# Optimization experiments

Hardware: AMD Instinct MI355X
Metric: run time of the kernel (lower is better)

The kernel has to match this reference:

```python
import jax, jax.numpy as jnp
import numpy as np
from jax import lax

START, STOP, NTAGS = 18, 19, 20
NEG = -10000.0
V, E, H, L = 100000, 300, 512, 512  # vocab, embed_dim, per-direction hidden, seq_len


def setup_inputs() -> dict:
    key = jax.random.key(0)
    ks = jax.random.split(key, 16)
    f = lambda k, s: jax.random.normal(k, s, dtype=jnp.float32) * 0.05
    trans = jax.random.normal(ks[14], (NTAGS, NTAGS), dtype=jnp.float32)
    trans = trans.at[START, :].set(NEG).at[:, STOP].set(NEG)
    return {
        "sentence": jax.random.randint(ks[0], (L,), 0, V),
        "embed_table": f(ks[1], (V, E)),
        "w_ih_f": f(ks[2], (4 * H, E)), "w_hh_f": f(ks[3], (4 * H, H)),
        "b_ih_f": f(ks[4], (4 * H,)), "b_hh_f": f(ks[5], (4 * H,)),
        "w_ih_b": f(ks[6], (4 * H, E)), "w_hh_b": f(ks[7], (4 * H, H)),
        "b_ih_b": f(ks[8], (4 * H,)), "b_hh_b": f(ks[9], (4 * H,)),
        "h0": f(ks[10], (2, H)), "c0": f(ks[11], (2, H)),
        "w_out": f(ks[12], (NTAGS, 2 * H)), "b_out": f(ks[13], (NTAGS,)),
        "transitions": trans,
    }


def _lstm_dir(x, wih, whh, bih, bhh, h0, c0, reverse):
    # x: [L, E]; PyTorch gate order i, f, g, o
    b = bih + bhh
    def step(carry, xt):
        h, c = carry
        g = xt @ wih.T + h @ whh.T + b  # [4H]
        i, fg, gg, o = jnp.split(g, 4)
        c = jax.nn.sigmoid(fg) * c + jax.nn.sigmoid(i) * jnp.tanh(gg)
        h = jax.nn.sigmoid(o) * jnp.tanh(c)
        return (h, c), h
    _, hs = lax.scan(step, (h0, c0), x, reverse=reverse)
    return hs  # [L, H] in time order


def _lstm_feats(sentence, embed_table, w_ih_f, w_hh_f, b_ih_f, b_hh_f,
                w_ih_b, w_hh_b, b_ih_b, b_hh_b, h0, c0, w_out, b_out):
    x = embed_table[sentence]  # [L, E]
    hf = _lstm_dir(x, w_ih_f, w_hh_f, b_ih_f, b_hh_f, h0[0], c0[0], False)
    hb = _lstm_dir(x, w_ih_b, w_hh_b, b_ih_b, b_hh_b, h0[1], c0[1], True)
    h = jnp.concatenate([hf, hb], axis=-1)  # [L, 2H]
    return h @ w_out.T + b_out  # [L, NTAGS]


def reference(sentence, embed_table, w_ih_f, w_hh_f, b_ih_f, b_hh_f,
              w_ih_b, w_hh_b, b_ih_b, b_hh_b, h0, c0, w_out, b_out, transitions):
    feats = _lstm_feats(sentence, embed_table, w_ih_f, w_hh_f, b_ih_f, b_hh_f,
                        w_ih_b, w_hh_b, b_ih_b, b_hh_b, h0, c0, w_out, b_out)
    init = jnp.full((NTAGS,), NEG, dtype=feats.dtype).at[START].set(0.0)

    def vstep(fv, feat):
        scores = fv[None, :] + transitions  # [next_tag, prev_tag]
        bptr = jnp.argmax(scores, axis=1)
        return jnp.max(scores, axis=1) + feat, bptr

    fv, bptrs = lax.scan(vstep, init, feats)  # bptrs: [L, NTAGS]
    terminal = fv + transitions[STOP]
    best = jnp.argmax(terminal)

    def back(tag, bp):
        # tag is the best tag at step t; bp maps tag_t -> tag_{t-1}
        return bp[tag], tag

    _, path = lax.scan(back, best, bptrs, reverse=True)  # [L] in time order
    return path
```

## Files before the change

kernel.cpp:

```cpp
#include <hip/hip_runtime.h>
#include <math.h>

#define L 512
#define E 300
#define H 512
#define G4H 2048
#define NTAGS 20
#define START_TAG 18
#define STOP_TAG 19

#define GPD 32
#define HPW 16
#define TR  16

#define OFF_XW    0u
#define OFF_HIST  8388608u
#define OFF_HBUF  10485760u
#define OFF_FEATS 10502144u

__global__ void k1_xw(const int* __restrict__ sentence,
                      const float* __restrict__ embed,
                      const float* __restrict__ wih_f, const float* __restrict__ wih_b,
                      const float* __restrict__ bih_f, const float* __restrict__ bhh_f,
                      const float* __restrict__ bih_b, const float* __restrict__ bhh_b,
                      float* __restrict__ xw) {
    int tid = threadIdx.x;
    int n   = blockIdx.x * 256 + tid;
    int t0  = blockIdx.y * TR;
    int dir = blockIdx.z;
    const float* wih = dir ? wih_b : wih_f;
    const float* bih = dir ? bih_b : bih_f;
    const float* bhh = dir ? bhh_b : bhh_f;
    const float* wrow = wih + (size_t)n * E;

    const float* xr[TR];
#pragma unroll
    for (int r = 0; r < TR; ++r)
        xr[r] = embed + (size_t)sentence[t0 + r] * E;

    float acc[TR];
#pragma unroll
    for (int r = 0; r < TR; ++r) acc[r] = 0.f;

    for (int kk = 0; kk < E / 4; ++kk) {
        float4 wv = ((const float4*)wrow)[kk];
#pragma unroll
        for (int r = 0; r < TR; ++r) {
            float4 xv = ((const float4*)xr[r])[kk];
            acc[r] = fmaf(wv.x, xv.x,
                     fmaf(wv.y, xv.y,
                     fmaf(wv.z, xv.z,
                     fmaf(wv.w, xv.w, acc[r]))));
        }
    }
    float b = bih[n] + bhh[n];
#pragma unroll
    for (int r = 0; r < TR; ++r)
        xw[((size_t)(dir * L) + (t0 + r)) * G4H + n] = acc[r] + b;
}

__global__ __launch_bounds__(512) void k2_lstm(
    const float* __restrict__ whh_f, const float* __restrict__ whh_b,
    const float* __restrict__ h0, const float* __restrict__ c0,
    const float* __restrict__ xw, float* __restrict__ hist,
    unsigned long long* __restrict__ hbuf) {
    const int bid = blockIdx.x;
    const int dir = bid >> 5;
    const int wg  = bid & 31;
    const int tid = threadIdx.x;
    const int wv  = tid >> 6;
    const int l   = tid & 63;
    const int gate = l >> 4;
    const int j    = l & 15;
    const int row  = gate * H + wg * HPW + j;

    const float* whh = dir ? whh_b : whh_f;
    const float* xwd = xw + (size_t)dir * L * G4H;
    float* histd = hist + (size_t)dir * L * H;
    unsigned long long* hb = hbuf + dir * 1024;

    float w[64];
    {
        const float* wp = whh + (size_t)row * H + wv * 64;
#pragma unroll
        for (int i = 0; i < 64; i += 4) {
            float4 v = *(const float4*)(wp + i);
            w[i] = v.x; w[i + 1] = v.y; w[i + 2] = v.z; w[i + 3] = v.w;
        }
    }

    __shared__ float pbuf[2][8][64];

    float c = (tid < HPW) ? c0[dir * H + wg * HPW + tid] : 0.f;

    for (int s = 1; s <= L; ++s) {
        const int t = dir ? (L - s) : (s - 1);
        float xg = xwd[(size_t)t * G4H + row];

        float hval;
        if (s == 1) {
            hval = h0[dir * H + tid];
        } else {
            unsigned long long* slot = hb + (((s - 1) & 1) << 9) + tid;
            unsigned long long u;
            while (((u = __hip_atomic_load(slot, __ATOMIC_RELAXED,
                                           __HIP_MEMORY_SCOPE_AGENT)) >> 32)
                   != (unsigned)(s - 1))
                __builtin_amdgcn_s_sleep(1);
            hval = __uint_as_float((unsigned)u);
        }

        float acc = 0.f;
#pragma unroll
        for (int i = 0; i < 64; ++i) {
            float hb_i = __uint_as_float(
                (unsigned)__builtin_amdgcn_readlane((int)__float_as_uint(hval), i));
            acc = fmaf(w[i], hb_i, acc);
        }
        pbuf[s & 1][wv][l] = acc;
        __syncthreads();

        if (tid < 64) {
            float g = 0.f;
#pragma unroll
            for (int p = 0; p < 8; ++p) g += pbuf[s & 1][p][l];
            float pre = g + xg;
            float a  = (gate == 2) ? 2.f * pre : pre;
            float sg = 1.f / (1.f + __expf(-a));
            float v  = (gate == 2) ? (2.f * sg - 1.f) : sg;
            float ig = __shfl(v, j);
            float fg = __shfl(v, j + 16);
            float gg = __shfl(v, j + 32);
            float og = __shfl(v, j + 48);
            if (tid < HPW) {
                c = fg * c + ig * gg;
                float tc = 2.f / (1.f + __expf(-2.f * c)) - 1.f;
                float h  = og * tc;
                histd[(size_t)t * H + wg * HPW + tid] = h;
                unsigned long long u =
                    ((unsigned long long)(unsigned)s << 32) |
                    (unsigned long long)__float_as_uint(h);
                __hip_atomic_store(hb + ((s & 1) << 9) + wg * HPW + tid, u,
                                   __ATOMIC_RELAXED, __HIP_MEMORY_SCOPE_AGENT);
            }
        }
    }
}

__global__ void k3_feats(const float* __restrict__ hist,
                         const float* __restrict__ wout,
                         const float* __restrict__ bout,
                         float* __restrict__ feats) {
    int t = blockIdx.x;
    int tid = threadIdx.x;
    int tag = tid >> 4;
    int part = tid & 15;
    const float* h0p = hist + (size_t)t * H;
    const float* h1p = hist + (size_t)L * H + (size_t)t * H;
    int j0 = part * 64;
    float acc = 0.f;
    for (int jj = 0; jj < 64; jj += 4) {
        int j = j0 + jj;
        float4 w4 = *(const float4*)(wout + (size_t)tag * (2 * H) + j);
        float4 h4 = (j < H) ? *(const float4*)(h0p + j)
                            : *(const float4*)(h1p + (j - H));
        acc = fmaf(w4.x, h4.x, fmaf(w4.y, h4.y,
              fmaf(w4.z, h4.z, fmaf(w4.w, h4.w, acc))));
    }
    acc += __shfl_xor(acc, 8, 16);
    acc += __shfl_xor(acc, 4, 16);
    acc += __shfl_xor(acc, 2, 16);
    acc += __shfl_xor(acc, 1, 16);
    if (part == 0) feats[(size_t)t * NTAGS + tag] = acc + bout[tag];
}

__global__ void k4_viterbi(const float* __restrict__ feats,
                           const float* __restrict__ trans,
                           int* __restrict__ out) {
    __shared__ unsigned char bp[L * NTAGS];
    int lane = threadIdx.x;
    bool act = lane < NTAGS;

    float trl[NTAGS];
#pragma unroll
    for (int p = 0; p < NTAGS; ++p)
        trl[p] = act ? trans[lane * NTAGS + p] : -1.0e30f;

    float fv = (lane == START_TAG) ? 0.f : -10000.f;
    float nf = act ? feats[lane] : 0.f;

    for (int t = 0; t < L; ++t) {
        float f = nf;
        if (act && t + 1 < L) nf = feats[(size_t)(t + 1) * NTAGS + lane];
        float best = -1.0e30f;
        int b = 0;
#pragma unroll
        for (int p = 0; p < NTAGS; ++p) {
            float sc = __shfl(fv, p) + trl[p];
            if (sc > best) { best = sc; b = p; }
        }
        fv = best + f;
        if (act) bp[t * NTAGS + lane] = (unsigned char)b;
    }

    float ts = act ? fv + trans[STOP_TAG * NTAGS + lane] : -1.0e30f;
    int bi = lane;
#pragma unroll
    for (int off = 32; off; off >>= 1) {
        float ov = __shfl_down(ts, off);
        int   oi = __shfl_down(bi, off);
        if (ov > ts) { ts = ov; bi = oi; }
    }
    if (lane == 0) {
        int tag = bi;
        out[L - 1] = tag;
        for (int t = L - 1; t >= 1; --t) {
            tag = bp[t * NTAGS + tag];
            out[t - 1] = tag;
        }
    }
}

extern "C" void kernel_launch(void* const* d_in, const int* in_sizes, int n_in,
                              void* d_out, int out_size, void* d_ws, size_t ws_size,
                              hipStream_t stream) {
    const int*   sentence = (const int*)d_in[0];
    const float* embed    = (const float*)d_in[1];
    const float* wih_f    = (const float*)d_in[2];
    const float* whh_f    = (const float*)d_in[3];
    const float* bih_f    = (const float*)d_in[4];
    const float* bhh_f    = (const float*)d_in[5];
    const float* wih_b    = (const float*)d_in[6];
    const float* whh_b    = (const float*)d_in[7];
    const float* bih_b    = (const float*)d_in[8];
    const float* bhh_b    = (const float*)d_in[9];
    const float* h0       = (const float*)d_in[10];
    const float* c0       = (const float*)d_in[11];
    const float* wout     = (const float*)d_in[12];
    const float* bout     = (const float*)d_in[13];
    const float* trans    = (const float*)d_in[14];
    int* out = (int*)d_out;

    char* ws = (char*)d_ws;
    float* xw    = (float*)(ws + OFF_XW);
    float* hist  = (float*)(ws + OFF_HIST);
    float* feats = (float*)(ws + OFF_FEATS);
    unsigned long long* hbuf = (unsigned long long*)(ws + OFF_HBUF);

    k1_xw<<<dim3(8, 32, 2), 256, 0, stream>>>(sentence, embed, wih_f, wih_b,
                                              bih_f, bhh_f, bih_b, bhh_b, xw);
    {
        void* args[] = {(void*)&whh_f, (void*)&whh_b, (void*)&h0, (void*)&c0,
                        (void*)&xw, (void*)&hist, (void*)&hbuf};
        hipLaunchCooperativeKernel((const void*)k2_lstm, dim3(2 * GPD), dim3(512),
                                   args, 0, stream);
    }
    k3_feats<<<L, 320, 0, stream>>>(hist, wout, bout, feats);
    k4_viterbi<<<1, 64, 0, stream>>>(feats, trans, out);
}
```

Before: 1.498 ms.

## Restructure LSTM recurrence into 256 single-wave blocks handling both directions

The recurrent kernel now uses 256 single-wavefront blocks. Each block owns two hidden units for both directions and keeps both directions' recurrent weights in registers. Hidden state is exchanged through tagged 64-bit slots polled in bulk, and the cross-wave shared-memory reduction and __syncthreads are replaced by in-wave shuffles. The input projection stages embeddings in shared memory with a smaller row tile and writes gate-interleaved output, and the Viterbi argmax becomes a tree reduction. The aim is to shorten the per-timestep critical path. The trade-offs are that every block now polls for all 512 hidden values per direction, and the cooperative launch is dropped, so co-residency of all 256 blocks is assumed rather than guaranteed.

```diff
diff --git a/kernel.cpp b/kernel.cpp
--- a/kernel.cpp
+++ b/kernel.cpp
@@ -1,5 +1,8 @@
 #include <hip/hip_runtime.h>
 #include <math.h>
+
+typedef unsigned long long u64;
+typedef unsigned int u32;
 
 #define L 512
 #define E 300
@@ -9,9 +12,7 @@
 #define START_TAG 18
 #define STOP_TAG 19
 
-#define GPD 32
-#define HPW 16
-#define TR  16
+#define TR 8
 
 #define OFF_XW    0u
 #define OFF_HIST  8388608u
@@ -24,6 +25,7 @@
                       const float* __restrict__ bih_f, const float* __restrict__ bhh_f,
                       const float* __restrict__ bih_b, const float* __restrict__ bhh_b,
                       float* __restrict__ xw) {
+    __shared__ float xs[TR][304];
     int tid = threadIdx.x;
     int n   = blockIdx.x * 256 + tid;
     int t0  = blockIdx.y * TR;
@@ -31,13 +33,13 @@
     const float* wih = dir ? wih_b : wih_f;
     const float* bih = dir ? bih_b : bih_f;
     const float* bhh = dir ? bhh_b : bhh_f;
+
+    for (int r = 0; r < TR; ++r)
+        for (int k = tid; k < E; k += 256)
+            xs[r][k] = embed[(size_t)sentence[t0 + r] * E + k];
+    __syncthreads();
+
     const float* wrow = wih + (size_t)n * E;
-
-    const float* xr[TR];
-#pragma unroll
-    for (int r = 0; r < TR; ++r)
-        xr[r] = embed + (size_t)sentence[t0 + r] * E;
-
     float acc[TR];
 #pragma unroll
     for (int r = 0; r < TR; ++r) acc[r] = 0.f;
@@ -46,103 +48,164 @@
         float4 wv = ((const float4*)wrow)[kk];
 #pragma unroll
         for (int r = 0; r < TR; ++r) {
-            float4 xv = ((const float4*)xr[r])[kk];
-            acc[r] = fmaf(wv.x, xv.x,
-                     fmaf(wv.y, xv.y,
-                     fmaf(wv.z, xv.z,
-                     fmaf(wv.w, xv.w, acc[r]))));
+            float4 xv = *(const float4*)(&xs[r][kk * 4]);
+            acc[r] = fmaf(wv.x, xv.x, fmaf(wv.y, xv.y,
+                     fmaf(wv.z, xv.z, fmaf(wv.w, xv.w, acc[r]))));
         }
     }
     float b = bih[n] + bhh[n];
+    int u = n & (H - 1), gate = n >> 9;
+    int pos = (u >> 1) * 8 + gate * 2 + (u & 1);
 #pragma unroll
     for (int r = 0; r < TR; ++r)
-        xw[((size_t)(dir * L) + (t0 + r)) * G4H + n] = acc[r] + b;
-}
-
-__global__ __launch_bounds__(512) void k2_lstm(
+        xw[((size_t)(dir * L) + (t0 + r)) * G4H + pos] = acc[r] + b;
+}
+
+__global__ __launch_bounds__(64) void k2_lstm(
     const float* __restrict__ whh_f, const float* __restrict__ whh_b,
     const float* __restrict__ h0, const float* __restrict__ c0,
     const float* __restrict__ xw, float* __restrict__ hist,
-    unsigned long long* __restrict__ hbuf) {
-    const int bid = blockIdx.x;
-    const int dir = bid >> 5;
-    const int wg  = bid & 31;
-    const int tid = threadIdx.x;
-    const int wv  = tid >> 6;
-    const int l   = tid & 63;
-    const int gate = l >> 4;
-    const int j    = l & 15;
-    const int row  = gate * H + wg * HPW + j;
-
-    const float* whh = dir ? whh_b : whh_f;
-    const float* xwd = xw + (size_t)dir * L * G4H;
-    float* histd = hist + (size_t)dir * L * H;
-    unsigned long long* hb = hbuf + dir * 1024;
-
-    float w[64];
+    u64* __restrict__ hbuf) {
+    const int g2 = blockIdx.x;
+    const int l  = threadIdx.x;
+    const int j  = l & 7;
+    const int q  = l >> 3;
+    const int u0 = g2 * 2;
+    const int row = (j >> 1) * H + u0 + (j & 1);
+
+    float w0[64], w1[64];
     {
-        const float* wp = whh + (size_t)row * H + wv * 64;
+        const float* p0 = whh_f + (size_t)row * H + q * 64;
+        const float* p1 = whh_b + (size_t)row * H + q * 64;
 #pragma unroll
         for (int i = 0; i < 64; i += 4) {
-            float4 v = *(const float4*)(wp + i);
-            w[i] = v.x; w[i + 1] = v.y; w[i + 2] = v.z; w[i + 3] = v.w;
-        }
-    }
-
-    __shared__ float pbuf[2][8][64];
-
-    float c = (tid < HPW) ? c0[dir * H + wg * HPW + tid] : 0.f;
+            float4 a = *(const float4*)(p0 + i);
+            w0[i] = a.x; w0[i+1] = a.y; w0[i+2] = a.z; w0[i+3] = a.w;
+            float4 b = *(const float4*)(p1 + i);
+            w1[i] = b.x; w1[i+1] = b.y; w1[i+2] = b.z; w1[i+3] = b.w;
+        }
+    }
+
+    __shared__ float hstage[2][8 * 68];
+
+    float c = 0.f;
+    if (l < 2)                 c = c0[u0 + l];
+    else if (l >= 8 && l < 10) c = c0[H + u0 + (l - 8)];
+
+    u64* hb0 = hbuf;
+    u64* hb1 = hbuf + 1024;
+    const int cons_base = l * 2;
+    const int prod_idx  = (g2 & 3) * 128 + (g2 >> 2) * 2;
 
     for (int s = 1; s <= L; ++s) {
-        const int t = dir ? (L - s) : (s - 1);
-        float xg = xwd[(size_t)t * G4H + row];
-
-        float hval;
+        const int t0 = s - 1, t1 = L - s;
+
+        float xwv = 0.f;
+        if (l < 16) {
+            int d = l >> 3;
+            xwv = xw[((size_t)(d * L + (d ? t1 : t0))) * G4H + g2 * 8 + (l & 7)];
+        }
+
+        float p0[8], p1[8];
         if (s == 1) {
-            hval = h0[dir * H + tid];
+            const float4* A = (const float4*)h0;
+            float4 a0 = A[2 * l], a1 = A[2 * l + 1];
+            p0[0]=a0.x; p0[1]=a0.y; p0[2]=a0.z; p0[3]=a0.w;
+            p0[4]=a1.x; p0[5]=a1.y; p0[6]=a1.z; p0[7]=a1.w;
+            const float4* B = (const float4*)(h0 + H);
+            float4 b0 = B[2 * l], b1 = B[2 * l + 1];
+            p1[0]=b0.x; p1[1]=b0.y; p1[2]=b0.z; p1[3]=b0.w;
+            p1[4]=b1.x; p1[5]=b1.y; p1[6]=b1.z; p1[7]=b1.w;
         } else {
-            unsigned long long* slot = hb + (((s - 1) & 1) << 9) + tid;
-            unsigned long long u;
-            while (((u = __hip_atomic_load(slot, __ATOMIC_RELAXED,
-                                           __HIP_MEMORY_SCOPE_AGENT)) >> 32)
-                   != (unsigned)(s - 1))
+            const u32 tag = (u32)(s - 1);
+            u64* b0 = hb0 + ((s - 1) & 1) * 512;
+            u64* b1 = hb1 + ((s - 1) & 1) * 512;
+            u64 v0[8], v1[8];
+#pragma unroll
+            for (int r = 0; r < 8; ++r)
+                v0[r] = __hip_atomic_load(b0 + (r >> 1) * 128 + cons_base + (r & 1),
+                                          __ATOMIC_RELAXED, __HIP_MEMORY_SCOPE_AGENT);
+#pragma unroll
+            for (int r = 0; r < 8; ++r)
+                v1[r] = __hip_atomic_load(b1 + (r >> 1) * 128 + cons_base + (r & 1),
+                                          __ATOMIC_RELAXED, __HIP_MEMORY_SCOPE_AGENT);
+            for (;;) {
+                bool ok = true;
+#pragma unroll
+                for (int r = 0; r < 8; ++r) ok &= ((u32)(v0[r] >> 32) == tag);
+                if (__all(ok)) break;
                 __builtin_amdgcn_s_sleep(1);
-            hval = __uint_as_float((unsigned)u);
-        }
-
-        float acc = 0.f;
-#pragma unroll
-        for (int i = 0; i < 64; ++i) {
-            float hb_i = __uint_as_float(
-                (unsigned)__builtin_amdgcn_readlane((int)__float_as_uint(hval), i));
-            acc = fmaf(w[i], hb_i, acc);
-        }
-        pbuf[s & 1][wv][l] = acc;
-        __syncthreads();
-
-        if (tid < 64) {
-            float g = 0.f;
-#pragma unroll
-            for (int p = 0; p < 8; ++p) g += pbuf[s & 1][p][l];
-            float pre = g + xg;
-            float a  = (gate == 2) ? 2.f * pre : pre;
-            float sg = 1.f / (1.f + __expf(-a));
-            float v  = (gate == 2) ? (2.f * sg - 1.f) : sg;
-            float ig = __shfl(v, j);
-            float fg = __shfl(v, j + 16);
-            float gg = __shfl(v, j + 32);
-            float og = __shfl(v, j + 48);
-            if (tid < HPW) {
-                c = fg * c + ig * gg;
-                float tc = 2.f / (1.f + __expf(-2.f * c)) - 1.f;
-                float h  = og * tc;
-                histd[(size_t)t * H + wg * HPW + tid] = h;
-                unsigned long long u =
-                    ((unsigned long long)(unsigned)s << 32) |
-                    (unsigned long long)__float_as_uint(h);
-                __hip_atomic_store(hb + ((s & 1) << 9) + wg * HPW + tid, u,
-                                   __ATOMIC_RELAXED, __HIP_MEMORY_SCOPE_AGENT);
+#pragma unroll
+                for (int r = 0; r < 8; ++r)
+                    v0[r] = __hip_atomic_load(b0 + (r >> 1) * 128 + cons_base + (r & 1),
+                                              __ATOMIC_RELAXED, __HIP_MEMORY_SCOPE_AGENT);
             }
+            for (;;) {
+                bool ok = true;
+#pragma unroll
+                for (int r = 0; r < 8; ++r) ok &= ((u32)(v1[r] >> 32) == tag);
+                if (__all(ok)) break;
+                __builtin_amdgcn_s_sleep(1);
+#pragma unroll
+                for (int r = 0; r < 8; ++r)
+                    v1[r] = __hip_atomic_load(b1 + (r >> 1) * 128 + cons_base + (r & 1),
+                                              __ATOMIC_RELAXED, __HIP_MEMORY_SCOPE_AGENT);
+            }
+#pragma unroll
+            for (int r = 0; r < 8; ++r) p0[r] = __uint_as_float((u32)v0[r]);
+#pragma unroll
+            for (int r = 0; r < 8; ++r) p1[r] = __uint_as_float((u32)v1[r]);
+        }
+
+        {
+            int wbase = q * 68 + 8 * j;
+            *(__shared__ float4*)&hstage[0][wbase]     = make_float4(p0[0], p0[1], p0[2], p0[3]);
+            *(__shared__ float4*)&hstage[0][wbase + 4] = make_float4(p0[4], p0[5], p0[6], p0[7]);
+            *(__shared__ float4*)&hstage[1][wbase]     = make_float4(p1[0], p1[1], p1[2], p1[3]);
+            *(__shared__ float4*)&hstage[1][wbase + 4] = make_float4(p1[4], p1[5], p1[6], p1[7]);
+        }
+
+        float acc0 = 0.f, acc1 = 0.f;
+#pragma unroll
+        for (int i = 0; i < 64; i += 4) {
+            float4 h4 = *(__shared__ float4*)&hstage[0][q * 68 + i];
+            acc0 = fmaf(w0[i], h4.x, fmaf(w0[i+1], h4.y,
+                   fmaf(w0[i+2], h4.z, fmaf(w0[i+3], h4.w, acc0))));
+            float4 g4 = *(__shared__ float4*)&hstage[1][q * 68 + i];
+            acc1 = fmaf(w1[i], g4.x, fmaf(w1[i+1], g4.y,
+                   fmaf(w1[i+2], g4.z, fmaf(w1[i+3], g4.w, acc1))));
+        }
+        acc0 += __shfl_xor(acc0, 8);  acc0 += __shfl_xor(acc0, 16); acc0 += __shfl_xor(acc0, 32);
+        acc1 += __shfl_xor(acc1, 8);  acc1 += __shfl_xor(acc1, 16); acc1 += __shfl_xor(acc1, 32);
+
+        float pre  = ((l < 8) ? acc0 : acc1) + xwv;
+        int   gate = (l & 7) >> 1;
+        float a2 = (gate == 2) ? 2.f * pre : pre;
+        float sg = 1.f / (1.f + __expf(-a2));
+        float vg = (gate == 2) ? (2.f * sg - 1.f) : sg;
+
+        float gi = __shfl(vg, (l & 8) + 0 + (l & 1));
+        float gf = __shfl(vg, (l & 8) + 2 + (l & 1));
+        float gg = __shfl(vg, (l & 8) + 4 + (l & 1));
+        float go = __shfl(vg, (l & 8) + 6 + (l & 1));
+        float hval = 0.f;
+        bool upd = (l < 2) || (l >= 8 && l < 10);
+        if (upd) {
+            c = gf * c + gi * gg;
+            float th = 2.f / (1.f + __expf(-2.f * c)) - 1.f;
+            hval = go * th;
+        }
+        float hnb = __shfl(hval, (l + 1) & 63);
+        if (l == 0 || l == 8) {
+            u64* bb = (l ? hb1 : hb0) + (s & 1) * 512 + prod_idx;
+            u64 e0 = ((u64)(u32)s << 32) | (u64)(u32)__float_as_uint(hval);
+            u64 e1 = ((u64)(u32)s << 32) | (u64)(u32)__float_as_uint(hnb);
+            __hip_atomic_store(bb,     e0, __ATOMIC_RELAXED, __HIP_MEMORY_SCOPE_AGENT);
+            __hip_atomic_store(bb + 1, e1, __ATOMIC_RELAXED, __HIP_MEMORY_SCOPE_AGENT);
+        }
+        if (upd) {
+            int d = l >> 3;
+            hist[((size_t)(d * L + (d ? t1 : t0))) * H + u0 + (l & 1)] = hval;
         }
     }
 }
@@ -192,15 +255,29 @@
     for (int t = 0; t < L; ++t) {
         float f = nf;
         if (act && t + 1 < L) nf = feats[(size_t)(t + 1) * NTAGS + lane];
-        float best = -1.0e30f;
-        int b = 0;
+        float tv[NTAGS];
+        int   ti[NTAGS];
 #pragma unroll
         for (int p = 0; p < NTAGS; ++p) {
-            float sc = __shfl(fv, p) + trl[p];
-            if (sc > best) { best = sc; b = p; }
-        }
-        fv = best + f;
-        if (act) bp[t * NTAGS + lane] = (unsigned char)b;
+            tv[p] = __shfl(fv, p) + trl[p];
+            ti[p] = p;
+        }
+#pragma unroll
+        for (int p = 0; p < 4; ++p) {
+            bool take = (tv[p + 16] > tv[p]) ||
+                        (tv[p + 16] == tv[p] && ti[p + 16] < ti[p]);
+            if (take) { tv[p] = tv[p + 16]; ti[p] = ti[p + 16]; }
+        }
+#pragma unroll
+        for (int w = 8; w >= 1; w >>= 1)
+#pragma unroll
+            for (int p = 0; p < 16; ++p) if (p < w) {
+                bool take = (tv[p + w] > tv[p]) ||
+                            (tv[p + w] == tv[p] && ti[p + w] < ti[p]);
+                if (take) { tv[p] = tv[p + w]; ti[p] = ti[p + w]; }
+            }
+        fv = tv[0] + f;
+        if (act) bp[t * NTAGS + lane] = (unsigned char)ti[0];
     }
 
     float ts = act ? fv + trans[STOP_TAG * NTAGS + lane] : -1.0e30f;
@@ -245,16 +322,11 @@
     float* xw    = (float*)(ws + OFF_XW);
     float* hist  = (float*)(ws + OFF_HIST);
     float* feats = (float*)(ws + OFF_FEATS);
-    unsigned long long* hbuf = (unsigned long long*)(ws + OFF_HBUF);
-
-    k1_xw<<<dim3(8, 32, 2), 256, 0, stream>>>(sentence, embed, wih_f, wih_b,
+    u64*   hbuf  = (u64*)(ws + OFF_HBUF);
+
+    k1_xw<<<dim3(8, 64, 2), 256, 0, stream>>>(sentence, embed, wih_f, wih_b,
                                               bih_f, bhh_f, bih_b, bhh_b, xw);
-    {
-        void* args[] = {(void*)&whh_f, (void*)&whh_b, (void*)&h0, (void*)&c0,
-                        (void*)&xw, (void*)&hist, (void*)&hbuf};
-        hipLaunchCooperativeKernel((const void*)k2_lstm, dim3(2 * GPD), dim3(512),
-                                   args, 0, stream);
-    }
+    k2_lstm<<<256, 64, 0, stream>>>(whh_f, whh_b, h0, c0, xw, hist, hbuf);
     k3_feats<<<L, 320, 0, stream>>>(hist, wout, bout, feats);
     k4_viterbi<<<1, 64, 0, stream>>>(feats, trans, out);
 }
```

After: 2.147 ms. 1.43x slower.

## Tile input GEMM in shared memory, restructure LSTM step reductions, tree-argmax Viterbi

Applied to the files above, without the earlier changes.

The input-projection kernel becomes a shared-memory tiled GEMM (64x64 tiles, 4x4 register blocking) and writes gates in a permuted layout. The recurrent kernel stages h in LDS, so each wave owns two hidden units and reduces the K split with wave shuffles. This removes the cross-wave pbuf sync and the serial single-wave gate stage. The Viterbi inner max becomes a tree reduction with tie-breaking, and the cooperative launch is replaced by a normal launch. That launch relies on all 64 blocks being co-resident, and it carries some risk if the permuted xw layout or the tie semantics are wrong.

```diff
diff --git a/kernel.cpp b/kernel.cpp
--- a/kernel.cpp
+++ b/kernel.cpp
@@ -1,5 +1,8 @@
 #include <hip/hip_runtime.h>
 #include <math.h>
+
+typedef unsigned long long u64;
+typedef unsigned int u32;
 
 #define L 512
 #define E 300
@@ -9,141 +12,184 @@
 #define START_TAG 18
 #define STOP_TAG 19
 
-#define GPD 32
-#define HPW 16
-#define TR  16
+#define KC 100
 
 #define OFF_XW    0u
 #define OFF_HIST  8388608u
 #define OFF_HBUF  10485760u
 #define OFF_FEATS 10502144u
 
-__global__ void k1_xw(const int* __restrict__ sentence,
-                      const float* __restrict__ embed,
-                      const float* __restrict__ wih_f, const float* __restrict__ wih_b,
-                      const float* __restrict__ bih_f, const float* __restrict__ bhh_f,
-                      const float* __restrict__ bih_b, const float* __restrict__ bhh_b,
-                      float* __restrict__ xw) {
-    int tid = threadIdx.x;
-    int n   = blockIdx.x * 256 + tid;
-    int t0  = blockIdx.y * TR;
-    int dir = blockIdx.z;
+__global__ __launch_bounds__(256) void k1_xw(
+    const int* __restrict__ sentence, const float* __restrict__ embed,
+    const float* __restrict__ wih_f, const float* __restrict__ wih_b,
+    const float* __restrict__ bih_f, const float* __restrict__ bhh_f,
+    const float* __restrict__ bih_b, const float* __restrict__ bhh_b,
+    float* __restrict__ xw) {
+    __shared__ float wST[KC][68];
+    __shared__ float xST[KC][68];
+    __shared__ int   sT[64];
+
+    const int tid = threadIdx.x;
+    const int tx = tid & 15;
+    const int ty = tid >> 4;
+    const int n_base = blockIdx.x * 64;
+    const int t_base = blockIdx.y * 64;
+    const int dir = blockIdx.z;
     const float* wih = dir ? wih_b : wih_f;
     const float* bih = dir ? bih_b : bih_f;
     const float* bhh = dir ? bhh_b : bhh_f;
-    const float* wrow = wih + (size_t)n * E;
-
-    const float* xr[TR];
-#pragma unroll
-    for (int r = 0; r < TR; ++r)
-        xr[r] = embed + (size_t)sentence[t0 + r] * E;
-
-    float acc[TR];
-#pragma unroll
-    for (int r = 0; r < TR; ++r) acc[r] = 0.f;
-
-    for (int kk = 0; kk < E / 4; ++kk) {
-        float4 wv = ((const float4*)wrow)[kk];
-#pragma unroll
-        for (int r = 0; r < TR; ++r) {
-            float4 xv = ((const float4*)xr[r])[kk];
-            acc[r] = fmaf(wv.x, xv.x,
-                     fmaf(wv.y, xv.y,
-                     fmaf(wv.z, xv.z,
-                     fmaf(wv.w, xv.w, acc[r]))));
-        }
-    }
-    float b = bih[n] + bhh[n];
-#pragma unroll
-    for (int r = 0; r < TR; ++r)
-        xw[((size_t)(dir * L) + (t0 + r)) * G4H + n] = acc[r] + b;
+
+    if (tid < 64) sT[tid] = sentence[t_base + tid];
+    __syncthreads();
+
+    float acc[4][4];
+#pragma unroll
+    for (int i = 0; i < 4; ++i)
+#pragma unroll
+        for (int j = 0; j < 4; ++j) acc[i][j] = 0.f;
+
+    for (int kc = 0; kc < E; kc += KC) {
+#pragma unroll
+        for (int i = 0; i < 25; ++i) {
+            int idx = i * 256 + tid;
+            int row = idx / KC, col = idx % KC;
+            wST[col][row] = wih[(size_t)(n_base + row) * E + kc + col];
+        }
+#pragma unroll
+        for (int i = 0; i < 25; ++i) {
+            int idx = i * 256 + tid;
+            int trow = idx / KC, col = idx % KC;
+            xST[col][trow] = embed[(size_t)sT[trow] * E + kc + col];
+        }
+        __syncthreads();
+
+#pragma unroll 4
+        for (int k = 0; k < KC; ++k) {
+            float4 wv4 = *(const float4*)&wST[k][ty * 4];
+            float4 xv4 = *(const float4*)&xST[k][tx * 4];
+            float wv[4] = {wv4.x, wv4.y, wv4.z, wv4.w};
+            float xv[4] = {xv4.x, xv4.y, xv4.z, xv4.w};
+#pragma unroll
+            for (int i = 0; i < 4; ++i)
+#pragma unroll
+                for (int j = 0; j < 4; ++j)
+                    acc[i][j] = fmaf(wv[i], xv[j], acc[i][j]);
+        }
+        __syncthreads();
+    }
+
+#pragma unroll
+    for (int i = 0; i < 4; ++i) {
+        int n = n_base + ty * 4 + i;
+        float b = bih[n] + bhh[n];
+        int u = n & (H - 1), g = n >> 9;
+        int pos = (u >> 4) * 64 + ((u & 15) >> 1) * 8 + g * 2 + (u & 1);
+#pragma unroll
+        for (int j = 0; j < 4; ++j) {
+            int t = t_base + tx * 4 + j;
+            xw[((size_t)(dir * L) + t) * G4H + pos] = acc[i][j] + b;
+        }
+    }
 }
 
 __global__ __launch_bounds__(512) void k2_lstm(
     const float* __restrict__ whh_f, const float* __restrict__ whh_b,
     const float* __restrict__ h0, const float* __restrict__ c0,
     const float* __restrict__ xw, float* __restrict__ hist,
-    unsigned long long* __restrict__ hbuf) {
+    u64* __restrict__ hbuf) {
     const int bid = blockIdx.x;
     const int dir = bid >> 5;
     const int wg  = bid & 31;
     const int tid = threadIdx.x;
     const int wv  = tid >> 6;
     const int l   = tid & 63;
-    const int gate = l >> 4;
-    const int j    = l & 15;
-    const int row  = gate * H + wg * HPW + j;
+    const int j   = l & 7;
+    const int q   = l >> 3;
+    const int g   = j >> 1;
+    const int p   = j & 1;
+    const int u0  = wg * 16;
+    const int unit = u0 + 2 * wv + p;
+    const int grow = g * H + unit;
 
     const float* whh = dir ? whh_b : whh_f;
-    const float* xwd = xw + (size_t)dir * L * G4H;
     float* histd = hist + (size_t)dir * L * H;
-    unsigned long long* hb = hbuf + dir * 1024;
+    u64* hb = hbuf + dir * 1024;
 
     float w[64];
     {
-        const float* wp = whh + (size_t)row * H + wv * 64;
+        const float* wp = whh + (size_t)grow * H + q * 64;
 #pragma unroll
         for (int i = 0; i < 64; i += 4) {
             float4 v = *(const float4*)(wp + i);
-            w[i] = v.x; w[i + 1] = v.y; w[i + 2] = v.z; w[i + 3] = v.w;
-        }
-    }
-
-    __shared__ float pbuf[2][8][64];
-
-    float c = (tid < HPW) ? c0[dir * H + wg * HPW + tid] : 0.f;
+            w[i] = v.x; w[i+1] = v.y; w[i+2] = v.z; w[i+3] = v.w;
+        }
+    }
+
+    __shared__ float hstage[2][8 * 68];
+
+    float c = 0.f;
+    if (l < 2) c = c0[dir * H + u0 + 2 * wv + l];
 
     for (int s = 1; s <= L; ++s) {
         const int t = dir ? (L - s) : (s - 1);
-        float xg = xwd[(size_t)t * G4H + row];
+        const int par = s & 1;
+
+        float xwv = 0.f;
+        if (l < 8)
+            xwv = xw[((size_t)(dir * L) + t) * G4H + wg * 64 + wv * 8 + j];
 
         float hval;
         if (s == 1) {
             hval = h0[dir * H + tid];
         } else {
-            unsigned long long* slot = hb + (((s - 1) & 1) << 9) + tid;
-            unsigned long long u;
+            u64* slot = hb + ((s - 1) & 1) * 512 + tid;
+            u64 u;
             while (((u = __hip_atomic_load(slot, __ATOMIC_RELAXED,
                                            __HIP_MEMORY_SCOPE_AGENT)) >> 32)
-                   != (unsigned)(s - 1))
+                   != (u32)(s - 1))
                 __builtin_amdgcn_s_sleep(1);
-            hval = __uint_as_float((unsigned)u);
-        }
+            hval = __uint_as_float((u32)u);
+        }
+        hstage[par][(tid >> 6) * 68 + (tid & 63)] = hval;
+        __syncthreads();
 
         float acc = 0.f;
-#pragma unroll
-        for (int i = 0; i < 64; ++i) {
-            float hb_i = __uint_as_float(
-                (unsigned)__builtin_amdgcn_readlane((int)__float_as_uint(hval), i));
-            acc = fmaf(w[i], hb_i, acc);
-        }
-        pbuf[s & 1][wv][l] = acc;
-        __syncthreads();
-
-        if (tid < 64) {
-            float g = 0.f;
-#pragma unroll
-            for (int p = 0; p < 8; ++p) g += pbuf[s & 1][p][l];
-            float pre = g + xg;
-            float a  = (gate == 2) ? 2.f * pre : pre;
-            float sg = 1.f / (1.f + __expf(-a));
-            float v  = (gate == 2) ? (2.f * sg - 1.f) : sg;
-            float ig = __shfl(v, j);
-            float fg = __shfl(v, j + 16);
-            float gg = __shfl(v, j + 32);
-            float og = __shfl(v, j + 48);
-            if (tid < HPW) {
-                c = fg * c + ig * gg;
-                float tc = 2.f / (1.f + __expf(-2.f * c)) - 1.f;
-                float h  = og * tc;
-                histd[(size_t)t * H + wg * HPW + tid] = h;
-                unsigned long long u =
-                    ((unsigned long long)(unsigned)s << 32) |
-                    (unsigned long long)__float_as_uint(h);
-                __hip_atomic_store(hb + ((s & 1) << 9) + wg * HPW + tid, u,
-                                   __ATOMIC_RELAXED, __HIP_MEMORY_SCOPE_AGENT);
-            }
-        }
+        const int base = q * 68;
+#pragma unroll
+        for (int i = 0; i < 64; i += 4) {
+            float4 h4 = *(__shared__ float4*)&hstage[par][base + i];
+            acc = fmaf(w[i], h4.x, fmaf(w[i+1], h4.y,
+                  fmaf(w[i+2], h4.z, fmaf(w[i+3], h4.w, acc))));
+        }
+        acc += __shfl_xor(acc, 8);
+        acc += __shfl_xor(acc, 16);
+        acc += __shfl_xor(acc, 32);
+
+        float pre = acc + xwv;
+        float a2 = (g == 2) ? 2.f * pre : pre;
+        float sg = 1.f / (1.f + __expf(-a2));
+        float vg = (g == 2) ? (2.f * sg - 1.f) : sg;
+
+        float gi = __shfl(vg, p);
+        float gf = __shfl(vg, 2 + p);
+        float gg = __shfl(vg, 4 + p);
+        float go = __shfl(vg, 6 + p);
+        float hout = 0.f;
+        if (l < 2) {
+            c = gf * c + gi * gg;
+            float th = 2.f / (1.f + __expf(-2.f * c)) - 1.f;
+            hout = go * th;
+        }
+        float h1 = __shfl(hout, 1);
+        if (l == 0) {
+            u64* bb = hb + par * 512 + u0 + 2 * wv;
+            u64 e0 = ((u64)(u32)s << 32) | (u64)__float_as_uint(hout);
+            u64 e1 = ((u64)(u32)s << 32) | (u64)__float_as_uint(h1);
+            __hip_atomic_store(bb,     e0, __ATOMIC_RELAXED, __HIP_MEMORY_SCOPE_AGENT);
+            __hip_atomic_store(bb + 1, e1, __ATOMIC_RELAXED, __HIP_MEMORY_SCOPE_AGENT);
+        }
+        if (l < 2)
+            histd[(size_t)t * H + u0 + 2 * wv + l] = hout;
     }
 }
 
@@ -192,15 +238,29 @@
     for (int t = 0; t < L; ++t) {
         float f = nf;
         if (act && t + 1 < L) nf = feats[(size_t)(t + 1) * NTAGS + lane];
-        float best = -1.0e30f;
-        int b = 0;
+        float tv[NTAGS];
+        int   ti[NTAGS];
 #pragma unroll
         for (int p = 0; p < NTAGS; ++p) {
-            float sc = __shfl(fv, p) + trl[p];
-            if (sc > best) { best = sc; b = p; }
-        }
-        fv = best + f;
-        if (act) bp[t * NTAGS + lane] = (unsigned char)b;
+            tv[p] = __shfl(fv, p) + trl[p];
+            ti[p] = p;
+        }
+#pragma unroll
+        for (int p = 0; p < 4; ++p) {
+            bool take = (tv[p + 16] > tv[p]) ||
+                        (tv[p + 16] == tv[p] && ti[p + 16] < ti[p]);
+            if (take) { tv[p] = tv[p + 16]; ti[p] = ti[p + 16]; }
+        }
+#pragma unroll
+        for (int w = 8; w >= 1; w >>= 1)
+#pragma unroll
+            for (int p = 0; p < 16; ++p) if (p < w) {
+                bool take = (tv[p + w] > tv[p]) ||
+                            (tv[p + w] == tv[p] && ti[p + w] < ti[p]);
+                if (take) { tv[p] = tv[p + w]; ti[p] = ti[p + w]; }
+            }
+        fv = tv[0] + f;
+        if (act) bp[t * NTAGS + lane] = (unsigned char)ti[0];
     }
 
     float ts = act ? fv + trans[STOP_TAG * NTAGS + lane] : -1.0e30f;
@@ -245,16 +305,11 @@
     float* xw    = (float*)(ws + OFF_XW);
     float* hist  = (float*)(ws + OFF_HIST);
     float* feats = (float*)(ws + OFF_FEATS);
-    unsigned long long* hbuf = (unsigned long long*)(ws + OFF_HBUF);
-
-    k1_xw<<<dim3(8, 32, 2), 256, 0, stream>>>(sentence, embed, wih_f, wih_b,
+    u64*   hbuf  = (u64*)(ws + OFF_HBUF);
+
+    k1_xw<<<dim3(32, 8, 2), 256, 0, stream>>>(sentence, embed, wih_f, wih_b,
                                               bih_f, bhh_f, bih_b, bhh_b, xw);
-    {
-        void* args[] = {(void*)&whh_f, (void*)&whh_b, (void*)&h0, (void*)&c0,
-                        (void*)&xw, (void*)&hist, (void*)&hbuf};
-        hipLaunchCooperativeKernel((const void*)k2_lstm, dim3(2 * GPD), dim3(512),
-                                   args, 0, stream);
-    }
+    k2_lstm<<<64, 512, 0, stream>>>(whh_f, whh_b, h0, c0, xw, hist, hbuf);
     k3_feats<<<L, 320, 0, stream>>>(hist, wout, bout, feats);
     k4_viterbi<<<1, 64, 0, stream>>>(feats, trans, out);
 }
```

Result: slower. 1.705 ms (+13.8%).
